# Kernel tuning notes

Hardware: AMD Instinct MI355X
Metric: run time of the kernel (lower is better)

The kernel has to match this reference:

```python
import jax, jax.numpy as jnp
import numpy as np

NUM_HEADS = 16
EMBED_DIM = 1024
INPUT_DIM = 1024
B, S = 4, 1024
MASK_VAL = -1e30  # fp32 branch of the original code


def setup_inputs() -> dict:
    key = jax.random.key(0)
    k1, k2, k3, k4 = jax.random.split(key, 4)
    x = jax.random.normal(k1, (B, S, INPUT_DIM), dtype=jnp.float32)
    mask = jax.random.randint(k2, (B, S), 0, 2, dtype=jnp.int32)
    # xavier_uniform-like init
    lim_qkv = float(np.sqrt(6.0 / (INPUT_DIM + 3 * EMBED_DIM)))
    lim_out = float(np.sqrt(6.0 / (EMBED_DIM + EMBED_DIM)))
    w_qkv = jax.random.uniform(k3, (3 * EMBED_DIM, INPUT_DIM), jnp.float32, -lim_qkv, lim_qkv)
    b_qkv = jnp.zeros((3 * EMBED_DIM,), jnp.float32)
    w_out = jax.random.uniform(k4, (EMBED_DIM, EMBED_DIM), jnp.float32, -lim_out, lim_out)
    b_out = jnp.zeros((EMBED_DIM,), jnp.float32)
    return {"x": x, "mask": mask, "w_qkv": w_qkv, "b_qkv": b_qkv,
            "w_out": w_out, "b_out": b_out}


def reference(x, mask, w_qkv, b_qkv, w_out, b_out):
    Bz, Sl, _ = x.shape
    Dh = EMBED_DIM // NUM_HEADS
    qkv = x @ w_qkv.T + b_qkv                       # (B,S,3E)
    q, k, v = jnp.split(qkv, 3, axis=-1)
    q = q.reshape(Bz, Sl, NUM_HEADS, Dh).transpose(0, 2, 1, 3)  # (B,H,S,Dh)
    k = k.reshape(Bz, Sl, NUM_HEADS, Dh).transpose(0, 2, 1, 3)
    v = v.reshape(Bz, Sl, NUM_HEADS, Dh).transpose(0, 2, 1, 3)
    energy = jnp.einsum('bhqd,bhkd->bhqk', q, k) / jnp.sqrt(jnp.float32(Dh))
    # Faithful reproduction of the original (buggy-looking) mask semantics:
    # positions with (k <= q) & (q < L_i) & (k < L_i) get filled with -1e30.
    L = mask.sum(axis=-1)                            # (B,)
    idx = jnp.arange(Sl)
    tri = idx[:, None] >= idx[None, :]               # (S,S): k <= q
    valid = idx[None, :] < L[:, None]                # (B,S)
    cond = tri[None, None] & valid[:, None, :, None] & valid[:, None, None, :]
    energy = jnp.where(cond, MASK_VAL, energy)
    attn = jax.nn.softmax(energy, axis=-1)           # (B,H,S,S)
    out = jnp.einsum('bhqk,bhkd->bhqd', attn, v)     # (B,H,S,Dh)
    out = out.transpose(0, 2, 1, 3).reshape(Bz, Sl, EMBED_DIM)
    return out @ w_out.T + b_out
```

## Files before the change

kernel.cpp:

```cpp
#include <hip/hip_runtime.h>


#define NHEADS 16
#define DHEAD  64
#define EDIM   1024
#define SLEN   1024
#define BATCH  4

typedef short bf16x8 __attribute__((ext_vector_type(8)));
typedef float f32x4  __attribute__((ext_vector_type(4)));
typedef float f32x16 __attribute__((ext_vector_type(16)));

#define MFMA_BF16(a,b,c) __builtin_amdgcn_mfma_f32_16x16x32_bf16((a),(b),(c),0,0,0)
#define MFMA32(a,b,c)    __builtin_amdgcn_mfma_f32_32x32x16_bf16((a),(b),(c),0,0,0)

typedef const __attribute__((address_space(1))) void gvoid_t;
typedef __attribute__((address_space(3))) void lvoid_t;

__device__ __forceinline__ unsigned short f2bf(float x) {
  union { float f; unsigned int u; } v; v.f = x;
  unsigned int r = v.u + 0x7fffu + ((v.u >> 16) & 1u);
  return (unsigned short)(r >> 16);
}

__device__ __forceinline__ unsigned pack2(float lo, float hi) {
  return (unsigned)f2bf(lo) | ((unsigned)f2bf(hi) << 16);
}

__device__ __forceinline__ void gl2lds16(const void* g, void* l) {
  __builtin_amdgcn_global_load_lds((gvoid_t*)g, (lvoid_t*)l, 16, 0, 0);
}

__global__ __launch_bounds__(256) void prep_cast(
    const float* __restrict__ x, const float* __restrict__ wq,
    const float* __restrict__ wo,
    unsigned short* __restrict__ xb, unsigned short* __restrict__ wqb,
    unsigned short* __restrict__ wob) {
  int i = blockIdx.x * 256 + threadIdx.x;
  const int NX  = BATCH * SLEN * EDIM / 4;
  const int NW1 = 3 * EDIM * EDIM / 4;
  const float4* src; unsigned short* dst; int j;
  if (i < NX)           { src = (const float4*)x;  dst = xb;  j = i; }
  else if (i < NX+NW1)  { src = (const float4*)wq; dst = wqb; j = i - NX; }
  else                  { src = (const float4*)wo; dst = wob; j = i - NX - NW1; }
  float4 v = src[j];
  ushort4 o;
  o.x = f2bf(v.x); o.y = f2bf(v.y); o.z = f2bf(v.z); o.w = f2bf(v.w);
  ((ushort4*)dst)[j] = o;
}

__global__ __launch_bounds__(256) void mask_sum(const int* __restrict__ mask,
                                                int* __restrict__ L) {
  int b = blockIdx.x;
  int t = threadIdx.x;
  int s = 0;
  for (int i = t; i < SLEN; i += 256) s += mask[b * SLEN + i];
  #pragma unroll
  for (int m = 1; m < 64; m <<= 1) s += __shfl_xor(s, m);
  __shared__ int part[4];
  if ((t & 63) == 0) part[t >> 6] = s;
  __syncthreads();
  if (t == 0) L[b] = part[0] + part[1] + part[2] + part[3];
}

template<int EPI>
__global__ __launch_bounds__(256) void gemm_bt(
    const unsigned short* __restrict__ A, const unsigned short* __restrict__ B,
    int M, int N, int K,
    const float* __restrict__ bias,
    float* __restrict__ outf,
    unsigned short* __restrict__ qb, unsigned short* __restrict__ kb,
    unsigned short* __restrict__ vb) {
  __shared__ __align__(16) unsigned short lds_a[128 * 32];
  __shared__ __align__(16) unsigned short lds_b[128 * 32];
  const int tid = threadIdx.x;
  const int w = tid >> 6, l = tid & 63;
  const int g = l >> 4, ln = l & 15;
  const int ntile = N >> 7;
  const int tm = blockIdx.x / ntile, tn = blockIdx.x % ntile;
  const int mBase = tm << 7, nBase = tn << 7;
  const int wr = w >> 1, wc = w & 1;

  f32x4 zz = {0.f, 0.f, 0.f, 0.f};
  f32x4 acc[4][4];
  #pragma unroll
  for (int m = 0; m < 4; ++m)
    #pragma unroll
    for (int n = 0; n < 4; ++n) acc[m][n] = zz;

  const int u0 = tid, u1 = tid + 256;
  const int r0 = u0 >> 2, c0 = (u0 & 3) << 3;
  const int r1 = u1 >> 2, c1 = (u1 & 3) << 3;
  const unsigned short* Ab = A + mBase * K;
  const unsigned short* Bb = B + nBase * K;
  unsigned short* da0 = &lds_a[(w * 64) * 8];
  unsigned short* da1 = &lds_a[(256 + w * 64) * 8];
  unsigned short* db0 = &lds_b[(w * 64) * 8];
  unsigned short* db1 = &lds_b[(256 + w * 64) * 8];

  for (int k0 = 0; k0 < K; k0 += 32) {
    gl2lds16(Ab + r0 * K + k0 + c0, da0);
    gl2lds16(Ab + r1 * K + k0 + c1, da1);
    gl2lds16(Bb + r0 * K + k0 + c0, db0);
    gl2lds16(Bb + r1 * K + k0 + c1, db1);
    __syncthreads();
    bf16x8 af[4], bfr[4];
    #pragma unroll
    for (int m = 0; m < 4; ++m)
      af[m] = *(const bf16x8*)&lds_a[(wr * 64 + m * 16 + ln) * 32 + g * 8];
    #pragma unroll
    for (int n = 0; n < 4; ++n)
      bfr[n] = *(const bf16x8*)&lds_b[(wc * 64 + n * 16 + ln) * 32 + g * 8];
    #pragma unroll
    for (int m = 0; m < 4; ++m)
      #pragma unroll
      for (int n = 0; n < 4; ++n)
        acc[m][n] = MFMA_BF16(af[m], bfr[n], acc[m][n]);
    __syncthreads();
  }

  #pragma unroll
  for (int m = 0; m < 4; ++m) {
    const int rowb = mBase + wr * 64 + m * 16 + g * 4;
    #pragma unroll
    for (int n = 0; n < 4; ++n) {
      const int col = nBase + wc * 64 + n * 16 + ln;
      const float bv = bias[col];
      #pragma unroll
      for (int r = 0; r < 4; ++r) {
        const float vv = acc[m][n][r] + bv;
        const int row = rowb + r;
        if (EPI == 0) {
          const int part = col >> 10;
          const int c = col & 1023;
          const int hh = c >> 6, d = c & 63;
          const int bb = row >> 10, s = row & 1023;
          const int bh = bb * NHEADS + hh;
          const unsigned short hv = f2bf(vv);
          if (part == 0)      qb[(bh * SLEN + s) * DHEAD + d] = hv;
          else if (part == 1) kb[(bh * SLEN + s) * DHEAD + d] = hv;
          else                vb[(bh * DHEAD + d) * SLEN + s] = hv;
        } else {
          outf[row * N + col] = vv;
        }
      }
    }
  }
}

__global__ __launch_bounds__(128) void attn(
    const unsigned short* __restrict__ qb, const unsigned short* __restrict__ kb,
    const unsigned short* __restrict__ vb, const int* __restrict__ Lp,
    unsigned short* __restrict__ yb) {
  const int bid = blockIdx.x;
  const int lid = (bid & 7) * 256 + (bid >> 3);
  const int bh = lid >> 5, qw = lid & 31;
  const int b = bh >> 4, h = bh & 15;
  const int L = Lp[b];
  const int tid = threadIdx.x;
  const int w = tid >> 6, l = tid & 63;
  const int l31 = l & 31, hi = l >> 5;
  const int q = qw * 32 + l31;

  const unsigned short* qp = qb + (size_t)bh * SLEN * DHEAD;
  const unsigned short* kp = kb + (size_t)bh * SLEN * DHEAD;
  const unsigned short* vp = vb + (size_t)bh * DHEAD * SLEN;

  bf16x8 qf[4];
  #pragma unroll
  for (int c = 0; c < 4; ++c)
    qf[c] = *(const bf16x8*)&qp[q * DHEAD + c * 16 + hi * 8];

  f32x16 o0 = {}; f32x16 o1 = {};
  float mrow = -__builtin_inff(), lrow = 0.f;
  const bool qv = q < L;
  const float C = 0.18033688011112042f;

  const bool allQ   = (qw * 32 + 31) < L;
  const bool noneQ  = (qw * 32) >= L;
  const bool skipOK = allQ && (L < SLEN);

  for (int t = w; t < 32; t += 2) {
    if (skipOK && t < qw) continue;
    const int kb0 = t * 32;
    f32x16 e = {};
    __builtin_amdgcn_s_setprio(1);
    #pragma unroll
    for (int c = 0; c < 4; ++c) {
      const bf16x8 kf = *(const bf16x8*)&kp[(kb0 + l31) * DHEAD + c * 16 + hi * 8];
      e = MFMA32(kf, qf[c], e);
    }
    __builtin_amdgcn_s_setprio(0);

    const bool domask = (!noneQ) && (t <= qw);
    float pm = -__builtin_inff();
    if (domask) {
      #pragma unroll
      for (int r = 0; r < 16; ++r) {
        const int key = kb0 + (r & 3) + 8 * (r >> 2) + 4 * hi;
        float s = e[r] * C;
        if (qv && (key <= q)) s = -1e30f;
        e[r] = s;
        pm = fmaxf(pm, s);
      }
    } else {
      #pragma unroll
      for (int r = 0; r < 16; ++r) {
        const float s = e[r] * C;
        e[r] = s;
        pm = fmaxf(pm, s);
      }
    }
    pm = fmaxf(pm, __shfl_xor(pm, 32));

    const bool need = !__all(pm <= mrow + 8.0f);
    if (need) {
      const float mn = fmaxf(mrow, pm);
      const float a = exp2f(mrow - mn);
      #pragma unroll
      for (int r = 0; r < 16; ++r) { o0[r] *= a; o1[r] *= a; }
      lrow *= a;
      mrow = mn;
    }
    float sum = 0.f;
    #pragma unroll
    for (int r = 0; r < 16; ++r) {
      const float pe = exp2f(e[r] - mrow);
      e[r] = pe; sum += pe;
    }
    sum += __shfl_xor(sum, 32);
    lrow += sum;

    bf16x8 pbf[2];
    #pragma unroll
    for (int kc = 0; kc < 2; ++kc) {
      const unsigned wA = pack2(e[8*kc+0], e[8*kc+1]);
      const unsigned wB = pack2(e[8*kc+2], e[8*kc+3]);
      const unsigned wC = pack2(e[8*kc+4], e[8*kc+5]);
      const unsigned wD = pack2(e[8*kc+6], e[8*kc+7]);
      const unsigned pA = __shfl_xor(wA, 32);
      const unsigned pB = __shfl_xor(wB, 32);
      const unsigned pC = __shfl_xor(wC, 32);
      const unsigned pD = __shfl_xor(wD, 32);
      union { unsigned u[4]; bf16x8 v; } pk;
      pk.u[0] = hi ? pC : wA;
      pk.u[1] = hi ? pD : wB;
      pk.u[2] = hi ? wC : pA;
      pk.u[3] = hi ? wD : pB;
      pbf[kc] = pk.v;
    }

    __builtin_amdgcn_s_setprio(1);
    #pragma unroll
    for (int kc = 0; kc < 2; ++kc) {
      const bf16x8 vf0 = *(const bf16x8*)&vp[l31 * SLEN + kb0 + kc * 16 + hi * 8];
      const bf16x8 vf1 = *(const bf16x8*)&vp[(32 + l31) * SLEN + kb0 + kc * 16 + hi * 8];
      o0 = MFMA32(vf0, pbf[kc], o0);
      o1 = MFMA32(vf1, pbf[kc], o1);
    }
    __builtin_amdgcn_s_setprio(0);
  }

  __shared__ float ml[2][2][32];
  __shared__ __align__(16) float obuf[64][34];
  if (hi == 0) { ml[w][0][l31] = mrow; ml[w][1][l31] = lrow; }
  if (w == 0) {
    #pragma unroll
    for (int r = 0; r < 16; ++r) obuf[l][16 + r] = o1[r];
  } else {
    #pragma unroll
    for (int r = 0; r < 16; ++r) obuf[l][r] = o0[r];
  }
  __syncthreads();
  const float m0 = ml[0][0][l31], m1 = ml[1][0][l31];
  const float l0 = ml[0][1][l31], l1 = ml[1][1][l31];
  const float mn = fmaxf(m0, m1);
  const float s0 = exp2f(m0 - mn), s1 = exp2f(m1 - mn);
  const float inv = 1.0f / (l0 * s0 + l1 * s1);
  unsigned short* yrow = yb + (size_t)(b * SLEN + q) * EDIM + h * DHEAD;
  if (w == 0) {
    #pragma unroll
    for (int rq = 0; rq < 4; ++rq) {
      ushort4 st;
      st.x = f2bf((o0[4*rq+0] * s0 + obuf[l][4*rq+0] * s1) * inv);
      st.y = f2bf((o0[4*rq+1] * s0 + obuf[l][4*rq+1] * s1) * inv);
      st.z = f2bf((o0[4*rq+2] * s0 + obuf[l][4*rq+2] * s1) * inv);
      st.w = f2bf((o0[4*rq+3] * s0 + obuf[l][4*rq+3] * s1) * inv);
      *(ushort4*)&yrow[8*rq + 4*hi] = st;
    }
  } else {
    #pragma unroll
    for (int rq = 0; rq < 4; ++rq) {
      ushort4 st;
      st.x = f2bf((obuf[l][16+4*rq+0] * s0 + o1[4*rq+0] * s1) * inv);
      st.y = f2bf((obuf[l][16+4*rq+1] * s0 + o1[4*rq+1] * s1) * inv);
      st.z = f2bf((obuf[l][16+4*rq+2] * s0 + o1[4*rq+2] * s1) * inv);
      st.w = f2bf((obuf[l][16+4*rq+3] * s0 + o1[4*rq+3] * s1) * inv);
      *(ushort4*)&yrow[32 + 8*rq + 4*hi] = st;
    }
  }
}

extern "C" void kernel_launch(void* const* d_in, const int* in_sizes, int n_in,
                              void* d_out, int out_size, void* d_ws, size_t ws_size,
                              hipStream_t stream) {
  const float* x    = (const float*)d_in[0];
  const int*   mask = (const int*)d_in[1];
  const float* wqkv = (const float*)d_in[2];
  const float* bqkv = (const float*)d_in[3];
  const float* wout = (const float*)d_in[4];
  const float* bout = (const float*)d_in[5];
  float* out = (float*)d_out;

  char* ws = (char*)d_ws;
  const size_t SZ_X   = (size_t)BATCH * SLEN * EDIM * 2;
  const size_t SZ_WQ  = (size_t)3 * EDIM * EDIM * 2;
  const size_t SZ_WO  = (size_t)EDIM * EDIM * 2;
  const size_t SZ_QKV = (size_t)BATCH * NHEADS * SLEN * DHEAD * 2;

  unsigned short* xb   = (unsigned short*)ws;               ws += SZ_X;
  unsigned short* wqb  = (unsigned short*)ws;               ws += SZ_WQ;
  unsigned short* wob  = (unsigned short*)ws;               ws += SZ_WO;
  unsigned short* qbuf = (unsigned short*)ws;               ws += SZ_QKV;
  unsigned short* kbuf = (unsigned short*)ws;               ws += SZ_QKV;
  unsigned short* vbuf = (unsigned short*)ws;               ws += SZ_QKV;
  unsigned short* ybuf = (unsigned short*)ws;               ws += SZ_X;
  int* Lbuf = (int*)ws;

  prep_cast<<<8192, 256, 0, stream>>>(x, wqkv, wout, xb, wqb, wob);
  mask_sum<<<BATCH, 256, 0, stream>>>(mask, Lbuf);
  gemm_bt<0><<<(4096 / 128) * (3072 / 128), 256, 0, stream>>>(
      xb, wqb, 4096, 3072, 1024, bqkv, nullptr, qbuf, kbuf, vbuf);
  attn<<<BATCH * NHEADS * (SLEN / 32), 128, 0, stream>>>(qbuf, kbuf, vbuf, Lbuf, ybuf);
  gemm_bt<1><<<(4096 / 128) * (1024 / 128), 256, 0, stream>>>(
      ybuf, wob, 4096, 1024, 1024, bout, out, nullptr, nullptr, nullptr);
}
```

Baseline: 244.9 us.

## Split attention key loop across four waves with K prefetch and LDS merge

```diff
diff --git a/kernel.cpp b/kernel.cpp
--- a/kernel.cpp
+++ b/kernel.cpp
@@ -148,7 +148,7 @@
   }
 }
 
-__global__ __launch_bounds__(128) void attn(
+__global__ __launch_bounds__(256) void attn(
     const unsigned short* __restrict__ qb, const unsigned short* __restrict__ kb,
     const unsigned short* __restrict__ vb, const int* __restrict__ Lp,
     unsigned short* __restrict__ yb) {
@@ -176,20 +176,35 @@
   const bool qv = q < L;
   const float C = 0.18033688011112042f;
 
-  const bool allQ   = (qw * 32 + 31) < L;
-  const bool noneQ  = (qw * 32) >= L;
-  const bool skipOK = allQ && (L < SLEN);
-
-  for (int t = w; t < 32; t += 2) {
-    if (skipOK && t < qw) continue;
+  const bool allQ  = (qw * 32 + 31) < L;
+  const bool noneQ = (qw * 32) >= L;
+  const int tstart = (allQ && L < SLEN) ? qw : 0;
+  const int tlo = tstart + ((w - tstart) & 3);
+
+  const int tp = tlo < 32 ? tlo : 31;
+  bf16x8 kcur[4];
+  #pragma unroll
+  for (int c = 0; c < 4; ++c)
+    kcur[c] = *(const bf16x8*)&kp[(tp * 32 + l31) * DHEAD + c * 16 + hi * 8];
+
+  for (int t = tlo; t < 32; t += 4) {
     const int kb0 = t * 32;
+    const int tn = (t + 4 < 32) ? (t + 4) : t;
+    bf16x8 knxt[4];
+    #pragma unroll
+    for (int c = 0; c < 4; ++c)
+      knxt[c] = *(const bf16x8*)&kp[(tn * 32 + l31) * DHEAD + c * 16 + hi * 8];
+    bf16x8 vf0[2], vf1[2];
+    #pragma unroll
+    for (int kc = 0; kc < 2; ++kc) {
+      vf0[kc] = *(const bf16x8*)&vp[l31 * SLEN + kb0 + kc * 16 + hi * 8];
+      vf1[kc] = *(const bf16x8*)&vp[(32 + l31) * SLEN + kb0 + kc * 16 + hi * 8];
+    }
+
     f32x16 e = {};
     __builtin_amdgcn_s_setprio(1);
     #pragma unroll
-    for (int c = 0; c < 4; ++c) {
-      const bf16x8 kf = *(const bf16x8*)&kp[(kb0 + l31) * DHEAD + c * 16 + hi * 8];
-      e = MFMA32(kf, qf[c], e);
-    }
+    for (int c = 0; c < 4; ++c) e = MFMA32(kcur[c], qf[c], e);
     __builtin_amdgcn_s_setprio(0);
 
     const bool domask = (!noneQ) && (t <= qw);
@@ -253,50 +268,73 @@
     __builtin_amdgcn_s_setprio(1);
     #pragma unroll
     for (int kc = 0; kc < 2; ++kc) {
-      const bf16x8 vf0 = *(const bf16x8*)&vp[l31 * SLEN + kb0 + kc * 16 + hi * 8];
-      const bf16x8 vf1 = *(const bf16x8*)&vp[(32 + l31) * SLEN + kb0 + kc * 16 + hi * 8];
-      o0 = MFMA32(vf0, pbf[kc], o0);
-      o1 = MFMA32(vf1, pbf[kc], o1);
+      o0 = MFMA32(vf0[kc], pbf[kc], o0);
+      o1 = MFMA32(vf1[kc], pbf[kc], o1);
     }
     __builtin_amdgcn_s_setprio(0);
-  }
-
-  __shared__ float ml[2][2][32];
-  __shared__ __align__(16) float obuf[64][34];
-  if (hi == 0) { ml[w][0][l31] = mrow; ml[w][1][l31] = lrow; }
+
+    #pragma unroll
+    for (int c = 0; c < 4; ++c) kcur[c] = knxt[c];
+  }
+
+  __shared__ float mls[4][2][32];
+  __shared__ __align__(16) float obuf[2][32][65];
+  if (hi == 0) { mls[w][0][l31] = mrow; mls[w][1][l31] = lrow; }
+  __syncthreads();
+  const float m0 = mls[0][0][l31], m1 = mls[1][0][l31];
+  const float m2 = mls[2][0][l31], m3 = mls[3][0][l31];
+  const float mstar = fmaxf(fmaxf(m0, m1), fmaxf(m2, m3));
+  const float denom = mls[0][1][l31] * exp2f(m0 - mstar)
+                    + mls[1][1][l31] * exp2f(m1 - mstar)
+                    + mls[2][1][l31] * exp2f(m2 - mstar)
+                    + mls[3][1][l31] * exp2f(m3 - mstar);
+  const float sw = exp2f(mrow - mstar) / denom;
+  #pragma unroll
+  for (int r = 0; r < 16; ++r) { o0[r] *= sw; o1[r] *= sw; }
+  if (w >= 2) {
+    #pragma unroll
+    for (int r = 0; r < 16; ++r) {
+      const int d = (r & 3) + 8 * (r >> 2) + 4 * hi;
+      obuf[w - 2][l31][d]      = o0[r];
+      obuf[w - 2][l31][d + 32] = o1[r];
+    }
+  }
+  __syncthreads();
+  if (w < 2) {
+    #pragma unroll
+    for (int r = 0; r < 16; ++r) {
+      const int d = (r & 3) + 8 * (r >> 2) + 4 * hi;
+      o0[r] += obuf[w][l31][d];
+      o1[r] += obuf[w][l31][d + 32];
+    }
+  }
+  __syncthreads();
+  if (w == 1) {
+    #pragma unroll
+    for (int r = 0; r < 16; ++r) {
+      const int d = (r & 3) + 8 * (r >> 2) + 4 * hi;
+      obuf[0][l31][d]      = o0[r];
+      obuf[0][l31][d + 32] = o1[r];
+    }
+  }
+  __syncthreads();
   if (w == 0) {
     #pragma unroll
-    for (int r = 0; r < 16; ++r) obuf[l][16 + r] = o1[r];
-  } else {
-    #pragma unroll
-    for (int r = 0; r < 16; ++r) obuf[l][r] = o0[r];
-  }
-  __syncthreads();
-  const float m0 = ml[0][0][l31], m1 = ml[1][0][l31];
-  const float l0 = ml[0][1][l31], l1 = ml[1][1][l31];
-  const float mn = fmaxf(m0, m1);
-  const float s0 = exp2f(m0 - mn), s1 = exp2f(m1 - mn);
-  const float inv = 1.0f / (l0 * s0 + l1 * s1);
-  unsigned short* yrow = yb + (size_t)(b * SLEN + q) * EDIM + h * DHEAD;
-  if (w == 0) {
+    for (int r = 0; r < 16; ++r) {
+      const int d = (r & 3) + 8 * (r >> 2) + 4 * hi;
+      o0[r] += obuf[0][l31][d];
+      o1[r] += obuf[0][l31][d + 32];
+    }
+    unsigned short* yrow = yb + (size_t)(b * SLEN + q) * EDIM + h * DHEAD;
     #pragma unroll
     for (int rq = 0; rq < 4; ++rq) {
-      ushort4 st;
-      st.x = f2bf((o0[4*rq+0] * s0 + obuf[l][4*rq+0] * s1) * inv);
-      st.y = f2bf((o0[4*rq+1] * s0 + obuf[l][4*rq+1] * s1) * inv);
-      st.z = f2bf((o0[4*rq+2] * s0 + obuf[l][4*rq+2] * s1) * inv);
-      st.w = f2bf((o0[4*rq+3] * s0 + obuf[l][4*rq+3] * s1) * inv);
-      *(ushort4*)&yrow[8*rq + 4*hi] = st;
-    }
-  } else {
-    #pragma unroll
-    for (int rq = 0; rq < 4; ++rq) {
-      ushort4 st;
-      st.x = f2bf((obuf[l][16+4*rq+0] * s0 + o1[4*rq+0] * s1) * inv);
-      st.y = f2bf((obuf[l][16+4*rq+1] * s0 + o1[4*rq+1] * s1) * inv);
-      st.z = f2bf((obuf[l][16+4*rq+2] * s0 + o1[4*rq+2] * s1) * inv);
-      st.w = f2bf((obuf[l][16+4*rq+3] * s0 + o1[4*rq+3] * s1) * inv);
-      *(ushort4*)&yrow[32 + 8*rq + 4*hi] = st;
+      ushort4 s0, s1;
+      s0.x = f2bf(o0[4*rq+0]); s0.y = f2bf(o0[4*rq+1]);
+      s0.z = f2bf(o0[4*rq+2]); s0.w = f2bf(o0[4*rq+3]);
+      s1.x = f2bf(o1[4*rq+0]); s1.y = f2bf(o1[4*rq+1]);
+      s1.z = f2bf(o1[4*rq+2]); s1.w = f2bf(o1[4*rq+3]);
+      *(ushort4*)&yrow[8*rq + 4*hi]      = s0;
+      *(ushort4*)&yrow[32 + 8*rq + 4*hi] = s1;
     }
   }
 }
@@ -331,7 +369,7 @@
   mask_sum<<<BATCH, 256, 0, stream>>>(mask, Lbuf);
   gemm_bt<0><<<(4096 / 128) * (3072 / 128), 256, 0, stream>>>(
       xb, wqb, 4096, 3072, 1024, bqkv, nullptr, qbuf, kbuf, vbuf);
-  attn<<<BATCH * NHEADS * (SLEN / 32), 128, 0, stream>>>(qbuf, kbuf, vbuf, Lbuf, ybuf);
+  attn<<<BATCH * NHEADS * (SLEN / 32), 256, 0, stream>>>(qbuf, kbuf, vbuf, Lbuf, ybuf);
   gemm_bt<1><<<(4096 / 128) * (1024 / 128), 256, 0, stream>>>(
       ybuf, wob, 4096, 1024, 1024, bout, out, nullptr, nullptr, nullptr);
 }
```

Measured after the change: 230.4 us. 5.9% less time.
